# Performance work log

Hardware: AMD Instinct MI355X
Metric: run time of the kernel (lower is better)

The kernel has to match this reference:

```python
import jax, jax.numpy as jnp
import numpy as np

V, D, NCTX, H, L, DM = 50257, 768, 1024, 12, 2, 3072
EPS = 1e-5
B, S = 2, 1024
DH = D // H


def _ln(x, w, b):
    # NOTE: faithful to source: divides by (std + eps), not sqrt(var + eps)
    m = jnp.mean(x, axis=-1, keepdims=True)
    std = jnp.sqrt(jnp.var(x, axis=-1, keepdims=True))
    return w * ((x - m) / (std + EPS)) + b


def setup_inputs() -> dict:
    key = jax.random.key(0)
    ks = jax.random.split(key, 20)
    r = 0.02
    inp = {
        "input_ids": jax.random.randint(ks[0], (B, S), 0, V),
        "embed": jax.random.normal(ks[1], (V, D), jnp.float32) * r,
        "pos_embed": jax.random.normal(ks[2], (NCTX, D), jnp.float32) * r,
        "ln1_w": jnp.ones((L, D)), "ln1_b": jnp.zeros((L, D)),
        "W_attn": jax.random.normal(ks[3], (L, 3 * D, D), jnp.float32) * r,
        "b_attn": jnp.zeros((L, 3 * D)),
        "W_O": jax.random.normal(ks[4], (L, D, D), jnp.float32) * r,
        "b_O": jnp.zeros((L, D)),
        "ln2_w": jnp.ones((L, D)), "ln2_b": jnp.zeros((L, D)),
        "W_in": jax.random.normal(ks[5], (L, DM, D), jnp.float32) * r,
        "b_in": jnp.zeros((L, DM)),
        "W_out": jax.random.normal(ks[6], (L, D, DM), jnp.float32) * r,
        "b_out": jnp.zeros((L, D)),
        "lnf_w": jnp.ones((D,)), "lnf_b": jnp.zeros((D,)),
        "W_U": jax.random.normal(ks[7], (V, D), jnp.float32) * r,
        "b_U": jnp.zeros((V,)),
    }
    return inp


def _forward(input_ids, embed, pos_embed, ln1_w, ln1_b, W_attn, b_attn, W_O, b_O,
             ln2_w, ln2_b, W_in, b_in, W_out, b_out, lnf_w, lnf_b, W_U, b_U):
    seq = input_ids.shape[1]
    res = embed[input_ids] + pos_embed[:seq][None, :, :]  # [B,S,D]
    causal = jnp.triu(jnp.ones((seq, seq), dtype=bool), 1)
    neg_inf = jnp.float32(-jnp.inf)
    for l in range(L):
        x = _ln(res, ln1_w[l], ln1_b[l])
        qkv = x @ W_attn[l].T + b_attn[l]  # [B,S,3D]
        q, k, v = jnp.split(qkv, 3, axis=-1)
        q = q.reshape(q.shape[0], seq, H, DH).transpose(0, 2, 1, 3)
        k = k.reshape(k.shape[0], seq, H, DH).transpose(0, 2, 1, 3)
        v = v.reshape(v.shape[0], seq, H, DH).transpose(0, 2, 1, 3)
        scores = jnp.einsum('bhqd,bhkd->bhqk', q, k) / (DH ** 0.5)
        scores = jnp.where(causal, neg_inf, scores)
        probs = jax.nn.softmax(scores, axis=-1)
        inter = jnp.einsum('bhqk,bhkd->bhqd', probs, v)
        inter = inter.transpose(0, 2, 1, 3).reshape(inter.shape[0], seq, D)
        res = inter @ W_O[l].T + b_O[l] + res
        y = _ln(res, ln2_w[l], ln2_b[l])
        h = jax.nn.gelu(y @ W_in[l].T + b_in[l], approximate=False)
        res = h @ W_out[l].T + b_out[l] + res
    res = _ln(res, lnf_w, lnf_b)
    return res @ W_U.T + b_U  # [B,S,V]


def reference(input_ids, embed, pos_embed, ln1_w, ln1_b, W_attn, b_attn, W_O, b_O,
              ln2_w, ln2_b, W_in, b_in, W_out, b_out, lnf_w, lnf_b, W_U, b_U):
    return _forward(input_ids, embed, pos_embed, ln1_w, ln1_b, W_attn, b_attn,
                    W_O, b_O, ln2_w, ln2_b, W_in, b_in, W_out, b_out,
                    lnf_w, lnf_b, W_U, b_U)
```

## Files before the change

### kernel.cpp

```cpp
#include <hip/hip_runtime.h>
#include <stdint.h>

#define D_MODEL 768
#define N_TOK   2048
#define SEQLEN  1024
#define N_HEAD  12
#define HEAD_D  64
#define N_LAYER 2
#define D_FF    3072
#define N_VOCAB 50257
#define D_QKV   2304

typedef unsigned short u16;
typedef __attribute__((ext_vector_type(8))) short bf16x8;
typedef __attribute__((ext_vector_type(4))) float f32x4;

__device__ __forceinline__ u16 f2b(float f) {
  uint32_t u = __float_as_uint(f);
  return (u16)((u + 0x7fffu + ((u >> 16) & 1u)) >> 16);
}
__device__ __forceinline__ float b2f(u16 h) {
  return __uint_as_float(((uint32_t)h) << 16);
}

__device__ __forceinline__ void gl2lds16(const void* g, void* l) {
  __builtin_amdgcn_global_load_lds(
      (const __attribute__((address_space(1))) uint32_t*)g,
      (__attribute__((address_space(3))) uint32_t*)l, 16, 0, 0);
}

__global__ __launch_bounds__(256) void cvt_k(const float* __restrict__ s,
                                             u16* __restrict__ d, int n4) {
  int i = blockIdx.x * 256 + threadIdx.x;
  if (i >= n4) return;
  float4 v = ((const float4*)s)[i];
  ushort4 o;
  o.x = f2b(v.x); o.y = f2b(v.y); o.z = f2b(v.z); o.w = f2b(v.w);
  ((ushort4*)d)[i] = o;
}

__global__ __launch_bounds__(256) void embed_k(const int* __restrict__ ids,
                                               const float* __restrict__ emb,
                                               const float* __restrict__ pos,
                                               float* __restrict__ R) {
  int t = blockIdx.x;
  int id = ids[t];
  int s = t & (SEQLEN - 1);
  const float* e = emb + (size_t)id * D_MODEL;
  const float* pp = pos + (size_t)s * D_MODEL;
  float* r = R + (size_t)t * D_MODEL;
  for (int i = threadIdx.x; i < D_MODEL; i += 256) r[i] = e[i] + pp[i];
}

__global__ __launch_bounds__(256) void ln_k(const float* __restrict__ X,
                                            const float* __restrict__ w,
                                            const float* __restrict__ b,
                                            u16* __restrict__ out) {
  int t = blockIdx.x;
  const float* x = X + (size_t)t * D_MODEL;
  float v0 = x[threadIdx.x], v1 = x[threadIdx.x + 256], v2 = x[threadIdx.x + 512];
  float s = v0 + v1 + v2;
  float s2 = v0 * v0 + v1 * v1 + v2 * v2;
  for (int off = 32; off; off >>= 1) {
    s  += __shfl_xor(s, off);
    s2 += __shfl_xor(s2, off);
  }
  __shared__ float rs[4], rq[4];
  int wv = threadIdx.x >> 6, ln = threadIdx.x & 63;
  if (ln == 0) { rs[wv] = s; rq[wv] = s2; }
  __syncthreads();
  s  = rs[0] + rs[1] + rs[2] + rs[3];
  s2 = rq[0] + rq[1] + rq[2] + rq[3];
  const float inv_d = 1.0f / (float)D_MODEL;
  float m = s * inv_d;
  float var = fmaxf(s2 * inv_d - m * m, 0.0f);
  float inv = 1.0f / (sqrtf(var) + 1e-5f);
  u16* o = out + (size_t)t * D_MODEL;
  int d0 = threadIdx.x;
  o[d0]       = f2b(w[d0]       * ((v0 - m) * inv) + b[d0]);
  o[d0 + 256] = f2b(w[d0 + 256] * ((v1 - m) * inv) + b[d0 + 256]);
  o[d0 + 512] = f2b(w[d0 + 512] * ((v2 - m) * inv) + b[d0 + 512]);
}

template <bool GELU, bool RES, bool OUT_BF16, bool VDUAL>
__global__ __launch_bounds__(256) void gemm_bt(
    const u16* __restrict__ A, const u16* __restrict__ B,
    const float* __restrict__ bias, const float* __restrict__ resid,
    void* __restrict__ Cout, u16* __restrict__ vtd, int M, int N, int K) {
  __shared__ u16 As[128 * 32];
  __shared__ u16 Bs[128 * 32];
  const int t = threadIdx.x;
  const int wv = t >> 6, ln = t & 63;
  const int wm = wv >> 1, wn = wv & 1;
  const int l15 = ln & 15, lq = ln >> 4;
  const int bm0 = blockIdx.y * 128;
  const int bn0 = blockIdx.x * 128;

  const int srow = wv * 32 + (ln >> 2);
  const int scol = (ln & 3) * 8;
  const u16* aS0 = A + (size_t)(bm0 + srow) * K + scol;
  const u16* aS1 = A + (size_t)(bm0 + srow + 16) * K + scol;
  int br0 = bn0 + srow;      if (br0 > N - 1) br0 = N - 1;
  int br1 = bn0 + srow + 16; if (br1 > N - 1) br1 = N - 1;
  const u16* bS0 = B + (size_t)br0 * K + scol;
  const u16* bS1 = B + (size_t)br1 * K + scol;
  u16* aD0 = &As[wv * 1024];
  u16* aD1 = &As[wv * 1024 + 512];
  u16* bD0 = &Bs[wv * 1024];
  u16* bD1 = &Bs[wv * 1024 + 512];

  f32x4 acc[4][4] = {};

  for (int kt = 0; kt < K; kt += 32) {
    gl2lds16(aS0 + kt, aD0);
    gl2lds16(aS1 + kt, aD1);
    gl2lds16(bS0 + kt, bD0);
    gl2lds16(bS1 + kt, bD1);
    __syncthreads();
    bf16x8 af[4], bfr[4];
#pragma unroll
    for (int mi = 0; mi < 4; ++mi)
      af[mi] = *(const bf16x8*)&As[(wm * 64 + mi * 16 + l15) * 32 + lq * 8];
#pragma unroll
    for (int ni = 0; ni < 4; ++ni)
      bfr[ni] = *(const bf16x8*)&Bs[(wn * 64 + ni * 16 + l15) * 32 + lq * 8];
#pragma unroll
    for (int mi = 0; mi < 4; ++mi)
#pragma unroll
      for (int ni = 0; ni < 4; ++ni)
        acc[mi][ni] = __builtin_amdgcn_mfma_f32_16x16x32_bf16(af[mi], bfr[ni],
                                                              acc[mi][ni], 0, 0, 0);
    __syncthreads();
  }

#pragma unroll
  for (int ni = 0; ni < 4; ++ni) {
    int col = bn0 + wn * 64 + ni * 16 + l15;
    if (col >= N) continue;
    float bv = bias[col];
#pragma unroll
    for (int mi = 0; mi < 4; ++mi) {
      uint32_t vlo = 0, vhi = 0;
#pragma unroll
      for (int r = 0; r < 4; ++r) {
        int row = bm0 + wm * 64 + mi * 16 + lq * 4 + r;
        float v = acc[mi][ni][r] + bv;
        if constexpr (RES) v += resid[(size_t)row * N + col];
        if constexpr (GELU) v = 0.5f * v * (1.0f + erff(v * 0.70710678118f));
        if constexpr (OUT_BF16) {
          u16 hv = f2b(v);
          ((u16*)Cout)[(size_t)row * N + col] = hv;
          if constexpr (VDUAL) {
            if (r < 2) vlo |= ((uint32_t)hv) << (16 * r);
            else       vhi |= ((uint32_t)hv) << (16 * (r - 2));
          }
        } else {
          ((float*)Cout)[(size_t)row * N + col] = v;
        }
      }
      if constexpr (VDUAL) {
        if (col >= 2 * D_MODEL) {
          int row0 = bm0 + wm * 64 + mi * 16 + lq * 4;
          int bq = row0 >> 10, s = row0 & 1023;
          uint2 pk; pk.x = vlo; pk.y = vhi;
          *(uint2*)(vtd + (((size_t)bq * D_MODEL + (col - 2 * D_MODEL)) << 10) + s) = pk;
        }
      }
    }
  }
}

__global__ __launch_bounds__(256) void attn_mfma_k(const u16* __restrict__ qkv,
                                                   const u16* __restrict__ vt,
                                                   u16* __restrict__ out) {
  const int bh = blockIdx.y;
  const int b = bh / N_HEAD, h = bh % N_HEAD;
  const int qt = (gridDim.x - 1) - blockIdx.x;
  const int w = threadIdx.x >> 6, ln = threadIdx.x & 63;
  const int l15 = ln & 15, lq = ln >> 4;
  const int q0 = qt * 64;
  const int qb = q0 + w * 16;

  __shared__ u16 Plds[4][1024];
  char* pbase = (char*)&Plds[w][0];

  const u16* qp = qkv + ((size_t)(b * SEQLEN + qb + l15)) * D_QKV + h * HEAD_D + lq * 8;
  bf16x8 qf[2];
#pragma unroll
  for (int dk = 0; dk < 2; ++dk) {
    uint4 raw = *(const uint4*)(qp + dk * 32);
    const u16* pr = (const u16*)&raw;
    bf16x8 f;
#pragma unroll
    for (int j = 0; j < 8; ++j) f[j] = (short)f2b(b2f(pr[j]) * 0.125f);
    qf[dk] = f;
  }

  f32x4 oacc[4] = {};
  float mrun = -1e30f, lsum = 0.0f;
  const int qg = qb + l15;
  const int nch = qt + 1;

  const u16* kbase = qkv + (size_t)b * SEQLEN * D_QKV + D_MODEL + h * HEAD_D;
  const u16* vbase = vt + ((size_t)(bh * 64 + l15)) * SEQLEN;

  for (int c = 0; c < nch; ++c) {
    const int k0 = c * 64;
    bf16x8 kf[4][2];
#pragma unroll
    for (int mt = 0; mt < 4; ++mt)
#pragma unroll
      for (int dk = 0; dk < 2; ++dk)
        kf[mt][dk] = *(const bf16x8*)(kbase + (size_t)(k0 + mt * 16 + l15) * D_QKV +
                                      dk * 32 + lq * 8);
    f32x4 st[4] = {};
#pragma unroll
    for (int mt = 0; mt < 4; ++mt)
#pragma unroll
      for (int dk = 0; dk < 2; ++dk)
        st[mt] = __builtin_amdgcn_mfma_f32_16x16x32_bf16(kf[mt][dk], qf[dk],
                                                         st[mt], 0, 0, 0);
    if (k0 + 63 > qb) {
#pragma unroll
      for (int mt = 0; mt < 4; ++mt)
#pragma unroll
        for (int r = 0; r < 4; ++r) {
          int kg = k0 + mt * 16 + lq * 4 + r;
          if (kg > qg) st[mt][r] = -1e30f;
        }
    }
    float mc = -1e30f;
#pragma unroll
    for (int mt = 0; mt < 4; ++mt)
#pragma unroll
      for (int r = 0; r < 4; ++r) mc = fmaxf(mc, st[mt][r]);
    mc = fmaxf(mc, __shfl_xor(mc, 16));
    mc = fmaxf(mc, __shfl_xor(mc, 32));
    float mnew = fmaxf(mrun, mc);
    float pscale = __expf(mrun - mnew);
    mrun = mnew;
    float psum = 0.0f;
#pragma unroll
    for (int mt = 0; mt < 4; ++mt) {
      float p0 = __expf(st[mt][0] - mnew);
      float p1 = __expf(st[mt][1] - mnew);
      float p2 = __expf(st[mt][2] - mnew);
      float p3 = __expf(st[mt][3] - mnew);
      psum += (p0 + p1) + (p2 + p3);
      uint2 pk;
      pk.x = (uint32_t)f2b(p0) | ((uint32_t)f2b(p1) << 16);
      pk.y = (uint32_t)f2b(p2) | ((uint32_t)f2b(p3) << 16);
      int ow = (l15 * 128 + mt * 32 + lq * 8) ^ ((l15 & 7) << 4);
      *(uint2*)(pbase + ow) = pk;
    }
    lsum = lsum * pscale + psum;
    float ps0 = __shfl(pscale, lq * 4 + 0);
    float ps1 = __shfl(pscale, lq * 4 + 1);
    float ps2 = __shfl(pscale, lq * 4 + 2);
    float ps3 = __shfl(pscale, lq * 4 + 3);
#pragma unroll
    for (int nt = 0; nt < 4; ++nt) {
      oacc[nt][0] *= ps0; oacc[nt][1] *= ps1;
      oacc[nt][2] *= ps2; oacc[nt][3] *= ps3;
    }
#pragma unroll
    for (int kc = 0; kc < 2; ++kc) {
      int orr = (l15 * 128 + kc * 64 + lq * 16) ^ ((l15 & 7) << 4);
      bf16x8 pf = *(const bf16x8*)(pbase + orr);
#pragma unroll
      for (int nt = 0; nt < 4; ++nt) {
        bf16x8 vf = *(const bf16x8*)(vbase + (size_t)nt * 16 * SEQLEN +
                                     k0 + kc * 32 + lq * 8);
        oacc[nt] = __builtin_amdgcn_mfma_f32_16x16x32_bf16(pf, vf, oacc[nt], 0, 0, 0);
      }
    }
  }
  lsum += __shfl_xor(lsum, 16);
  lsum += __shfl_xor(lsum, 32);
  float inv = 1.0f / lsum;
  float i0 = __shfl(inv, lq * 4 + 0);
  float i1 = __shfl(inv, lq * 4 + 1);
  float i2 = __shfl(inv, lq * 4 + 2);
  float i3 = __shfl(inv, lq * 4 + 3);
  u16* ob = out + ((size_t)(b * SEQLEN + qb + lq * 4)) * D_MODEL + h * HEAD_D + l15;
#pragma unroll
  for (int nt = 0; nt < 4; ++nt) {
    ob[(size_t)0 * D_MODEL + nt * 16] = f2b(oacc[nt][0] * i0);
    ob[(size_t)1 * D_MODEL + nt * 16] = f2b(oacc[nt][1] * i1);
    ob[(size_t)2 * D_MODEL + nt * 16] = f2b(oacc[nt][2] * i2);
    ob[(size_t)3 * D_MODEL + nt * 16] = f2b(oacc[nt][3] * i3);
  }
}

extern "C" void kernel_launch(void* const* d_in, const int* in_sizes, int n_in,
                              void* d_out, int out_size, void* d_ws, size_t ws_size,
                              hipStream_t stream) {
  (void)in_sizes; (void)n_in; (void)out_size; (void)ws_size;
  const int*   ids   = (const int*)d_in[0];
  const float* emb   = (const float*)d_in[1];
  const float* pos   = (const float*)d_in[2];
  const float* ln1w  = (const float*)d_in[3];
  const float* ln1b  = (const float*)d_in[4];
  const float* Wattn = (const float*)d_in[5];
  const float* battn = (const float*)d_in[6];
  const float* WO    = (const float*)d_in[7];
  const float* bO    = (const float*)d_in[8];
  const float* ln2w  = (const float*)d_in[9];
  const float* ln2b  = (const float*)d_in[10];
  const float* Win   = (const float*)d_in[11];
  const float* bin   = (const float*)d_in[12];
  const float* Wout  = (const float*)d_in[13];
  const float* bout  = (const float*)d_in[14];
  const float* lnfw  = (const float*)d_in[15];
  const float* lnfb  = (const float*)d_in[16];
  const float* WU    = (const float*)d_in[17];
  const float* bU    = (const float*)d_in[18];

  char* p = (char*)d_ws;
  auto carve = [&](size_t bytes) {
    char* r = p;
    p += (bytes + 255) & ~(size_t)255;
    return r;
  };
  float* R      = (float*)carve((size_t)N_TOK * D_MODEL * 4);
  u16*   xb     = (u16*)carve((size_t)N_TOK * D_MODEL * 2);
  u16*   qkvb   = (u16*)carve((size_t)N_TOK * D_QKV * 2);
  u16*   attnb  = (u16*)carve((size_t)N_TOK * D_MODEL * 2);
  u16*   hb     = (u16*)carve((size_t)N_TOK * D_FF * 2);
  u16*   vtb    = (u16*)carve((size_t)2 * D_MODEL * SEQLEN * 2);
  u16*   Wattnb = (u16*)carve((size_t)N_LAYER * D_QKV * D_MODEL * 2);
  u16*   WOb    = (u16*)carve((size_t)N_LAYER * D_MODEL * D_MODEL * 2);
  u16*   Winb   = (u16*)carve((size_t)N_LAYER * D_FF * D_MODEL * 2);
  u16*   Woutb  = (u16*)carve((size_t)N_LAYER * D_MODEL * D_FF * 2);
  u16*   WUb    = (u16*)carve((size_t)N_VOCAB * D_MODEL * 2);

  auto cvt = [&](const float* s, u16* d, size_t n) {
    int n4 = (int)(n / 4);
    cvt_k<<<dim3((n4 + 255) / 256), dim3(256), 0, stream>>>(s, d, n4);
  };
  cvt(Wattn, Wattnb, (size_t)N_LAYER * D_QKV * D_MODEL);
  cvt(WO,    WOb,    (size_t)N_LAYER * D_MODEL * D_MODEL);
  cvt(Win,   Winb,   (size_t)N_LAYER * D_FF * D_MODEL);
  cvt(Wout,  Woutb,  (size_t)N_LAYER * D_MODEL * D_FF);
  cvt(WU,    WUb,    (size_t)N_VOCAB * D_MODEL);

  embed_k<<<dim3(N_TOK), dim3(256), 0, stream>>>(ids, emb, pos, R);

  for (int l = 0; l < N_LAYER; ++l) {
    ln_k<<<dim3(N_TOK), dim3(256), 0, stream>>>(R, ln1w + l * D_MODEL, ln1b + l * D_MODEL, xb);
    gemm_bt<false, false, true, true><<<dim3(D_QKV / 128, N_TOK / 128), 256, 0, stream>>>(
        xb, Wattnb + (size_t)l * D_QKV * D_MODEL, battn + l * D_QKV, nullptr,
        qkvb, vtb, N_TOK, D_QKV, D_MODEL);
    attn_mfma_k<<<dim3(SEQLEN / 64, 2 * N_HEAD), 256, 0, stream>>>(qkvb, vtb, attnb);
    gemm_bt<false, true, false, false><<<dim3(D_MODEL / 128, N_TOK / 128), 256, 0, stream>>>(
        attnb, WOb + (size_t)l * D_MODEL * D_MODEL, bO + l * D_MODEL, R,
        R, nullptr, N_TOK, D_MODEL, D_MODEL);
    ln_k<<<dim3(N_TOK), dim3(256), 0, stream>>>(R, ln2w + l * D_MODEL, ln2b + l * D_MODEL, xb);
    gemm_bt<true, false, true, false><<<dim3(D_FF / 128, N_TOK / 128), 256, 0, stream>>>(
        xb, Winb + (size_t)l * D_FF * D_MODEL, bin + l * D_FF, nullptr,
        hb, nullptr, N_TOK, D_FF, D_MODEL);
    gemm_bt<false, true, false, false><<<dim3(D_MODEL / 128, N_TOK / 128), 256, 0, stream>>>(
        hb, Woutb + (size_t)l * D_MODEL * D_FF, bout + l * D_MODEL, R,
        R, nullptr, N_TOK, D_MODEL, D_FF);
  }
  ln_k<<<dim3(N_TOK), dim3(256), 0, stream>>>(R, lnfw, lnfb, xb);
  gemm_bt<false, false, false, false><<<dim3((N_VOCAB + 127) / 128, N_TOK / 128), 256, 0, stream>>>(
      xb, WUb, bU, nullptr, d_out, nullptr, N_TOK, N_VOCAB, D_MODEL);
}
```

Before: 1.359 ms.

## Double-buffer GEMM LDS tiles and remap workgroups per XCD for L2 reuse

The bf16 MFMA GEMM now keeps two LDS buffers for the A and B tiles, so the global-to-LDS copy of the next K slice is issued before the current slice's MFMAs. This hides load latency behind compute at the cost of twice the shared memory per block, which can lower occupancy. Launches switch to a 1D grid with an XCD-aware remap. Consecutive tiles on the same XCD walk down M for a fixed N column, so the weight tile, including the large vocabulary projection, is reused in that XCD's L2.

```diff
diff --git a/kernel.cpp b/kernel.cpp
--- a/kernel.cpp
+++ b/kernel.cpp
@@ -87,14 +87,21 @@
     const u16* __restrict__ A, const u16* __restrict__ B,
     const float* __restrict__ bias, const float* __restrict__ resid,
     void* __restrict__ Cout, u16* __restrict__ vtd, int M, int N, int K) {
-  __shared__ u16 As[128 * 32];
-  __shared__ u16 Bs[128 * 32];
+  __shared__ u16 As[2][128 * 32];
+  __shared__ u16 Bs[2][128 * 32];
   const int t = threadIdx.x;
   const int wv = t >> 6, ln = t & 63;
   const int wm = wv >> 1, wn = wv & 1;
   const int l15 = ln & 15, lq = ln >> 4;
-  const int bm0 = blockIdx.y * 128;
-  const int bn0 = blockIdx.x * 128;
+
+  const int mtiles = M >> 7;
+  const int nwg = gridDim.x;
+  const int bid = blockIdx.x;
+  const int qc = nwg >> 3, rc = nwg & 7;
+  const int xcd = bid & 7, lid = bid >> 3;
+  const int wgid = (xcd < rc ? xcd * (qc + 1) : rc * (qc + 1) + (xcd - rc) * qc) + lid;
+  const int bm0 = (wgid % mtiles) * 128;
+  const int bn0 = (wgid / mtiles) * 128;
 
   const int srow = wv * 32 + (ln >> 2);
   const int scol = (ln & 3) * 8;
@@ -104,26 +111,33 @@
   int br1 = bn0 + srow + 16; if (br1 > N - 1) br1 = N - 1;
   const u16* bS0 = B + (size_t)br0 * K + scol;
   const u16* bS1 = B + (size_t)br1 * K + scol;
-  u16* aD0 = &As[wv * 1024];
-  u16* aD1 = &As[wv * 1024 + 512];
-  u16* bD0 = &Bs[wv * 1024];
-  u16* bD1 = &Bs[wv * 1024 + 512];
 
   f32x4 acc[4][4] = {};
-
-  for (int kt = 0; kt < K; kt += 32) {
-    gl2lds16(aS0 + kt, aD0);
-    gl2lds16(aS1 + kt, aD1);
-    gl2lds16(bS0 + kt, bD0);
-    gl2lds16(bS1 + kt, bD1);
-    __syncthreads();
+  const int nk = K >> 5;
+
+  gl2lds16(aS0, &As[0][wv * 1024]);
+  gl2lds16(aS1, &As[0][wv * 1024 + 512]);
+  gl2lds16(bS0, &Bs[0][wv * 1024]);
+  gl2lds16(bS1, &Bs[0][wv * 1024 + 512]);
+  __syncthreads();
+
+  for (int kt = 0; kt < nk; ++kt) {
+    const int cur = kt & 1;
+    if (kt + 1 < nk) {
+      const int ko = (kt + 1) << 5;
+      const int nx = cur ^ 1;
+      gl2lds16(aS0 + ko, &As[nx][wv * 1024]);
+      gl2lds16(aS1 + ko, &As[nx][wv * 1024 + 512]);
+      gl2lds16(bS0 + ko, &Bs[nx][wv * 1024]);
+      gl2lds16(bS1 + ko, &Bs[nx][wv * 1024 + 512]);
+    }
     bf16x8 af[4], bfr[4];
 #pragma unroll
     for (int mi = 0; mi < 4; ++mi)
-      af[mi] = *(const bf16x8*)&As[(wm * 64 + mi * 16 + l15) * 32 + lq * 8];
+      af[mi] = *(const bf16x8*)&As[cur][(wm * 64 + mi * 16 + l15) * 32 + lq * 8];
 #pragma unroll
     for (int ni = 0; ni < 4; ++ni)
-      bfr[ni] = *(const bf16x8*)&Bs[(wn * 64 + ni * 16 + l15) * 32 + lq * 8];
+      bfr[ni] = *(const bf16x8*)&Bs[cur][(wn * 64 + ni * 16 + l15) * 32 + lq * 8];
 #pragma unroll
     for (int mi = 0; mi < 4; ++mi)
 #pragma unroll
@@ -346,24 +360,25 @@
 
   embed_k<<<dim3(N_TOK), dim3(256), 0, stream>>>(ids, emb, pos, R);
 
+  const int MT = N_TOK / 128;
   for (int l = 0; l < N_LAYER; ++l) {
     ln_k<<<dim3(N_TOK), dim3(256), 0, stream>>>(R, ln1w + l * D_MODEL, ln1b + l * D_MODEL, xb);
-    gemm_bt<false, false, true, true><<<dim3(D_QKV / 128, N_TOK / 128), 256, 0, stream>>>(
+    gemm_bt<false, false, true, true><<<dim3((D_QKV / 128) * MT), 256, 0, stream>>>(
         xb, Wattnb + (size_t)l * D_QKV * D_MODEL, battn + l * D_QKV, nullptr,
         qkvb, vtb, N_TOK, D_QKV, D_MODEL);
     attn_mfma_k<<<dim3(SEQLEN / 64, 2 * N_HEAD), 256, 0, stream>>>(qkvb, vtb, attnb);
-    gemm_bt<false, true, false, false><<<dim3(D_MODEL / 128, N_TOK / 128), 256, 0, stream>>>(
+    gemm_bt<false, true, false, false><<<dim3((D_MODEL / 128) * MT), 256, 0, stream>>>(
         attnb, WOb + (size_t)l * D_MODEL * D_MODEL, bO + l * D_MODEL, R,
         R, nullptr, N_TOK, D_MODEL, D_MODEL);
     ln_k<<<dim3(N_TOK), dim3(256), 0, stream>>>(R, ln2w + l * D_MODEL, ln2b + l * D_MODEL, xb);
-    gemm_bt<true, false, true, false><<<dim3(D_FF / 128, N_TOK / 128), 256, 0, stream>>>(
+    gemm_bt<true, false, true, false><<<dim3((D_FF / 128) * MT), 256, 0, stream>>>(
         xb, Winb + (size_t)l * D_FF * D_MODEL, bin + l * D_FF, nullptr,
         hb, nullptr, N_TOK, D_FF, D_MODEL);
-    gemm_bt<false, true, false, false><<<dim3(D_MODEL / 128, N_TOK / 128), 256, 0, stream>>>(
+    gemm_bt<false, true, false, false><<<dim3((D_MODEL / 128) * MT), 256, 0, stream>>>(
         hb, Woutb + (size_t)l * D_MODEL * D_FF, bout + l * D_MODEL, R,
         R, nullptr, N_TOK, D_MODEL, D_FF);
   }
   ln_k<<<dim3(N_TOK), dim3(256), 0, stream>>>(R, lnfw, lnfb, xb);
-  gemm_bt<false, false, false, false><<<dim3((N_VOCAB + 127) / 128, N_TOK / 128), 256, 0, stream>>>(
+  gemm_bt<false, false, false, false><<<dim3(((N_VOCAB + 127) / 128) * MT), 256, 0, stream>>>(
       xb, WUb, bU, nullptr, d_out, nullptr, N_TOK, N_VOCAB, D_MODEL);
 }
```

Result: no change. 1.368 ms (+0.7%).
